# Optimization experiments

Hardware: AMD Instinct MI355X
Metric: run time of the kernel (lower is better)

## Reference

```python
import jax, jax.numpy as jnp
import numpy as np

B, N, C = 2, 2048, 1024
H = 16
HD = C // H  # 64


def setup_inputs() -> dict:
    key = jax.random.key(0)
    ks = jax.random.split(key, 6)
    x = jax.random.normal(ks[0], (B, N, C), dtype=jnp.float32)
    # realistic rotary angles
    inv_freq = 1.0 / (10000.0 ** (np.arange(0, HD, 2, dtype=np.float32) / HD))
    t = np.arange(N, dtype=np.float32)
    freqs = np.outer(t, inv_freq)                      # [N, HD/2]
    emb = np.concatenate([freqs, freqs], axis=-1)      # [N, HD]
    cos = jnp.asarray(np.cos(emb), dtype=jnp.float32)
    sin = jnp.asarray(np.sin(emb), dtype=jnp.float32)
    qkv_w = jax.random.normal(ks[1], (3 * C, C), dtype=jnp.float32) * (1.0 / np.sqrt(C))
    proj_w = jax.random.normal(ks[2], (C, C), dtype=jnp.float32) * (1.0 / np.sqrt(C))
    proj_b = jnp.zeros((C,), dtype=jnp.float32)
    return {"x": x, "cos": cos, "sin": sin, "qkv_w": qkv_w, "proj_w": proj_w, "proj_b": proj_b}


def _apply_rope(x, cos, sin):
    # x: [B, H, N, HD]; cos/sin: [N, HD] (broadcast over B, H)
    x1, x2 = jnp.split(x, 2, axis=-1)
    rotated = jnp.concatenate([-x2, x1], axis=-1)
    return x * cos + rotated * sin


def reference(x, cos, sin, qkv_w, proj_w, proj_b):
    b, n, c = x.shape
    scale = (c // H) ** (-0.5)
    qkv = jnp.einsum('bnc,dc->bnd', x, qkv_w)          # [B, N, 3C]
    qkv = qkv.reshape(b, n, 3, H, HD).transpose(2, 0, 3, 1, 4)  # [3, B, H, N, HD]
    q, k, v = qkv[0], qkv[1], qkv[2]
    q = _apply_rope(q, cos, sin)
    k = _apply_rope(k, cos, sin)
    attn = jnp.einsum('bhid,bhjd->bhij', q, k) * scale  # [B, H, N, N]
    attn = jax.nn.softmax(attn, axis=-1)
    out = jnp.einsum('bhij,bhjd->bhid', attn, v)        # [B, H, N, HD]
    out = out.transpose(0, 2, 1, 3).reshape(b, n, c)    # [B, N, C]
    return jnp.einsum('bnc,dc->bnd', out, proj_w) + proj_b
```

## Files before the change

### kernel.cpp

```cpp
#include <hip/hip_runtime.h>
#include <stdint.h>

typedef __bf16 bf16;
typedef bf16 bf16x8 __attribute__((ext_vector_type(8)));
typedef float f32x4 __attribute__((ext_vector_type(4)));
typedef float f32x16 __attribute__((ext_vector_type(16)));
typedef unsigned short u16x8 __attribute__((ext_vector_type(8)));
typedef unsigned short u16x4 __attribute__((ext_vector_type(4)));

__device__ __forceinline__ unsigned short f2bfu(float f) {
    union { bf16 h; unsigned short u; } x;
    x.h = (bf16)f;
    return x.u;
}
__device__ __forceinline__ float bfu2f(unsigned short u) {
    union { unsigned int i; float f; } x;
    x.i = ((unsigned int)u) << 16;
    return x.f;
}
__device__ __forceinline__ unsigned int pack2bf(float a, float b) {
    union { bf16 h[2]; unsigned int u; } x;
    x.h[0] = (bf16)a; x.h[1] = (bf16)b;
    return x.u;
}
__device__ __forceinline__ void pl32_swap(unsigned int &a, unsigned int &b) {
    asm volatile("v_permlane32_swap_b32 %0, %1" : "+v"(a), "+v"(b));
}

__device__ __forceinline__ void gld_lds16(const void* g, void* l) {
    __builtin_amdgcn_global_load_lds(
        (const __attribute__((address_space(1))) unsigned int*)(uintptr_t)g,
        (__attribute__((address_space(3))) unsigned int*)(unsigned int)(uintptr_t)l,
        16, 0, 0);
}

__global__ void cast_bf16_kernel(const float* __restrict__ in,
                                 unsigned short* __restrict__ out, int n8) {
    int i = blockIdx.x * blockDim.x + threadIdx.x;
    if (i >= n8) return;
    const f32x4* p = (const f32x4*)(in + (size_t)i * 8);
    f32x4 a = p[0], b = p[1];
    u16x8 o;
    o[0]=f2bfu(a[0]); o[1]=f2bfu(a[1]); o[2]=f2bfu(a[2]); o[3]=f2bfu(a[3]);
    o[4]=f2bfu(b[0]); o[5]=f2bfu(b[1]); o[6]=f2bfu(b[2]); o[7]=f2bfu(b[3]);
    *(u16x8*)(out + (size_t)i * 8) = o;
}

__global__ void rope_kernel(unsigned short* __restrict__ qkv,
                            const float* __restrict__ cosp,
                            const float* __restrict__ sinp) {
    int tid = blockIdx.x * blockDim.x + threadIdx.x;
    int i8  = tid & 3;
    int h   = (tid >> 2) & 15;
    int sel = (tid >> 6) & 1;
    int n   = (tid >> 7) & 2047;
    int b   = tid >> 18;
    size_t base = ((size_t)(b*2048 + n))*3072 + sel*1024 + h*64 + i8*8;
    u16x8 x1 = *(u16x8*)(qkv + base);
    u16x8 x2 = *(u16x8*)(qkv + base + 32);
    const f32x4* cp = (const f32x4*)(cosp + n*64 + i8*8);
    const f32x4* sp = (const f32x4*)(sinp + n*64 + i8*8);
    f32x4 c0 = cp[0], c1 = cp[1], s0 = sp[0], s1 = sp[1];
    float scale = sel ? 1.0f : (0.125f * 1.44269504088896f);
    u16x8 o1, o2;
#pragma unroll
    for (int j = 0; j < 8; j++) {
        float cc = (j < 4) ? c0[j] : c1[j-4];
        float ss = (j < 4) ? s0[j] : s1[j-4];
        float a = bfu2f(x1[j]), d = bfu2f(x2[j]);
        o1[j] = f2bfu((a*cc - d*ss) * scale);
        o2[j] = f2bfu((d*cc + a*ss) * scale);
    }
    *(u16x8*)(qkv + base)      = o1;
    *(u16x8*)(qkv + base + 32) = o2;
}

__global__ __launch_bounds__(512, 2) void gemm_qkv8(
    const unsigned short* __restrict__ A, const unsigned short* __restrict__ B,
    unsigned short* __restrict__ C, int M, int N, int K)
{
    extern __shared__ char smem[];
    int nwgx = gridDim.x;
    int nwg  = nwgx * gridDim.y;
    int orig = blockIdx.y * nwgx + blockIdx.x;
    int cpx  = nwg >> 3;
    int wg   = (orig & 7) * cpx + (orig >> 3);
    int bx = wg % nwgx, by = wg / nwgx;
    int m0 = by << 8, n0 = bx << 8;
    int t  = threadIdx.x;
    int wv = t >> 6, l = t & 63;
    int fr = l & 15, fq = l >> 4;
    int wm = (wv >> 2) << 7;
    int wn = (wv & 3) << 6;
    int aswz = (fr & 3) << 4;

    auto stage = [&](int kt, int bsel) {
        int k0 = kt << 5;
        char* base = smem + (bsel << 15);
#pragma unroll
        for (int j = 0; j < 2; ++j) {
            int y   = (j << 13) + t * 16;
            int ly  = y ^ (((y >> 6) & 3) << 4);
            int row = ly >> 6;
            int colu = (ly & 63) >> 1;
            gld_lds16(A + (size_t)(m0 + row) * K + k0 + colu,
                      base + ((j << 13) + (wv << 10)));
            gld_lds16(B + (size_t)(n0 + row) * K + k0 + colu,
                      base + 16384 + ((j << 13) + (wv << 10)));
        }
    };

    f32x4 acc[8][4];
#pragma unroll
    for (int m = 0; m < 8; ++m)
#pragma unroll
        for (int n = 0; n < 4; ++n) acc[m][n] = f32x4{0.f, 0.f, 0.f, 0.f};

    stage(0, 0);
    stage(1, 1);
    int cb = 0;
    for (int kt = 0; kt < 32; ++kt) {
        if (kt < 31) asm volatile("s_waitcnt vmcnt(4)" ::: "memory");
        else         asm volatile("s_waitcnt vmcnt(0)" ::: "memory");
        __builtin_amdgcn_s_barrier();
        if (kt + 2 < 32) {
            int sb = cb - 1; if (sb < 0) sb = 2;
            stage(kt + 2, sb);
        }
        const char* base = smem + (cb << 15);
        const char* Ab = base + ((wm + fr) << 6) + ((fq * 16) ^ aswz);
        const char* Bb = base + 16384 + ((wn + fr) << 6) + ((fq * 16) ^ aswz);
        bf16x8 bfr[4], af[4];
#pragma unroll
        for (int n = 0; n < 4; ++n) bfr[n] = *(const bf16x8*)(Bb + (n << 10));
#pragma unroll
        for (int m = 0; m < 4; ++m) af[m]  = *(const bf16x8*)(Ab + (m << 10));
        __builtin_amdgcn_s_barrier();
        __builtin_amdgcn_s_setprio(1);
#pragma unroll
        for (int m = 0; m < 4; ++m)
#pragma unroll
            for (int n = 0; n < 4; ++n)
                acc[m][n] = __builtin_amdgcn_mfma_f32_16x16x32_bf16(af[m], bfr[n], acc[m][n], 0, 0, 0);
        __builtin_amdgcn_s_setprio(0);
#pragma unroll
        for (int m = 0; m < 4; ++m) af[m] = *(const bf16x8*)(Ab + ((m + 4) << 10));
        __builtin_amdgcn_s_barrier();
        __builtin_amdgcn_s_setprio(1);
#pragma unroll
        for (int m = 0; m < 4; ++m)
#pragma unroll
            for (int n = 0; n < 4; ++n)
                acc[m + 4][n] = __builtin_amdgcn_mfma_f32_16x16x32_bf16(af[m], bfr[n], acc[m + 4][n], 0, 0, 0);
        __builtin_amdgcn_s_setprio(0);
        cb = (cb == 2) ? 0 : cb + 1;
    }
#pragma unroll
    for (int m = 0; m < 8; ++m)
#pragma unroll
        for (int n = 0; n < 4; ++n)
#pragma unroll
            for (int e = 0; e < 4; ++e) {
                int row = m0 + wm + m * 16 + fq * 4 + e;
                int col = n0 + wn + n * 16 + fr;
                C[(size_t)row * N + col] = f2bfu(acc[m][n][e]);
            }
}

template<int OUT_F32>
__global__ __launch_bounds__(256, 2) void gemm_bt(
    const unsigned short* __restrict__ A, const unsigned short* __restrict__ B,
    void* __restrict__ Cp, const float* __restrict__ bias,
    int M, int N, int K)
{
    __shared__ __align__(16) unsigned short As[2][128*32];
    __shared__ __align__(16) unsigned short Bs[2][128*32];
    int nwg  = gridDim.x * gridDim.y;
    int orig = blockIdx.y * gridDim.x + blockIdx.x;
    int qq = nwg >> 3, rr = nwg & 7;
    int xcd = orig & 7, idx = orig >> 3;
    int wg = (xcd < rr) ? (xcd*(qq+1) + idx) : (rr*(qq+1) + (xcd-rr)*qq + idx);
    int bx = wg % gridDim.x, by = wg / gridDim.x;
    int m0 = by * 128, n0 = bx * 128;
    int t = threadIdx.x;
    int w = t >> 6, l = t & 63;
    int c = l & 15, g = l >> 4;
    int wm = (w >> 1) * 64, wn = (w & 1) * 64;

    auto stage = [&](int kt, int bsel) {
#pragma unroll
        for (int r2 = 0; r2 < 2; ++r2) {
            int xb = w*2048 + r2*1024;
            int x  = xb + l*16;
            int row  = x >> 6;
            int colu = (x & 63) >> 1;
            int k0 = kt << 5;
            gld_lds16(A + (size_t)(m0+row)*K + k0 + colu, (void*)(As[bsel] + (xb >> 1)));
            gld_lds16(B + (size_t)(n0+row)*K + k0 + colu, (void*)(Bs[bsel] + (xb >> 1)));
        }
    };

    f32x4 acc[4][4];
#pragma unroll
    for (int i = 0; i < 4; i++)
#pragma unroll
        for (int j = 0; j < 4; j++) acc[i][j] = f32x4{0.f,0.f,0.f,0.f};

    int nkt = K >> 5;
    stage(0, 0);
    int cur = 0;
    for (int kt = 0; kt < nkt; ++kt) {
        __syncthreads();
        if (kt + 1 < nkt) stage(kt + 1, cur ^ 1);
        const unsigned short* Ab = As[cur] + wm*32;
        const unsigned short* Bb = Bs[cur] + wn*32;
        bf16x8 af[4], bfr[4];
#pragma unroll
        for (int i = 0; i < 4; i++) af[i]  = *(const bf16x8*)(Ab + (i*16+c)*32 + g*8);
#pragma unroll
        for (int i = 0; i < 4; i++) bfr[i] = *(const bf16x8*)(Bb + (i*16+c)*32 + g*8);
#pragma unroll
        for (int i = 0; i < 4; i++)
#pragma unroll
            for (int j = 0; j < 4; j++)
                acc[i][j] = __builtin_amdgcn_mfma_f32_16x16x32_bf16(af[i], bfr[j], acc[i][j], 0, 0, 0);
        cur ^= 1;
    }
#pragma unroll
    for (int i = 0; i < 4; i++)
#pragma unroll
        for (int j = 0; j < 4; j++)
#pragma unroll
            for (int e = 0; e < 4; e++) {
                int row = m0 + wm + i*16 + g*4 + e;
                int col = n0 + wn + j*16 + c;
                float v = acc[i][j][e];
                if (bias) v += bias[col];
                if (OUT_F32) ((float*)Cp)[(size_t)row*N + col] = v;
                else ((unsigned short*)Cp)[(size_t)row*N + col] = f2bfu(v);
            }
}

__global__ __launch_bounds__(512, 4) void attn_kernel(
    const unsigned short* __restrict__ qkv, unsigned short* __restrict__ outp)
{
    __shared__ __align__(16) char lds[65536];
    int bh = blockIdx.y;
    int b = bh >> 4, h = bh & 15;
    int q0 = blockIdx.x << 7;
    int t = threadIdx.x;
    int w = t >> 6, l = t & 63;
    int pair = w >> 2, wp = w & 3;
    int tp = t & 255;
    int q = l & 31, hi = l >> 5;
    int qw = q0 + wp*32;
    size_t bh_base = ((size_t)b*2048)*3072 + (size_t)h*64;

    auto kbase = [&](int bsel) -> char* { return lds + (((pair << 1) | bsel) << 13); };
    auto vbase = [&](int bsel) -> char* { return lds + 32768 + (((pair << 1) | bsel) << 13); };

    auto stageK = [&](int kv0, int bsel) {
#pragma unroll
        for (int r2 = 0; r2 < 2; ++r2) {
            int xb = wp*2048 + r2*1024;
            int x  = xb + l*16;
            int row  = x >> 7;
            int scolb = (x & 127) ^ ((row & 7) << 4);
            gld_lds16(qkv + bh_base + 1024 + (size_t)(kv0 + row)*3072 + (scolb >> 1),
                      kbase(bsel) + xb);
        }
    };
    auto loadV = [&](int kv0, u16x8 &v0, u16x8 &v1) {
        int p  = tp >> 3;
        int hb = (tp & 7) << 3;
        const unsigned short* src = qkv + bh_base + 2048 + (size_t)(kv0 + 2*p)*3072 + hb;
        v0 = *(const u16x8*)src;
        v1 = *(const u16x8*)(src + 3072);
    };
    auto writeV = [&](const u16x8 &v0, const u16x8 &v1, int bsel) {
        int p  = tp >> 3;
        int hb = (tp & 7) << 3;
        char* vb = vbase(bsel);
#pragma unroll
        for (int e = 0; e < 8; e++) {
            int hd = hb + e;
            int colb = (4*p) ^ ((((hd) ^ (hd >> 3)) & 7) << 4);
            *(unsigned int*)(vb + hd*128 + colb) =
                (unsigned int)v0[e] | ((unsigned int)v1[e] << 16);
        }
    };

    bf16x8 qf[4];
#pragma unroll
    for (int dc = 0; dc < 4; dc++)
        qf[dc] = *(const bf16x8*)(qkv + bh_base + (size_t)(qw + q)*3072 + dc*16 + hi*8);

    f32x16 oacc[2];
#pragma unroll
    for (int e = 0; e < 16; e++) { oacc[0][e] = 0.f; oacc[1][e] = 0.f; }
    float lsum = 0.f;

    int tile0 = pair << 4;
    u16x8 vc0, vc1, vn0, vn1;
    stageK(tile0 << 6, 0);
    loadV(tile0 << 6, vc0, vc1);
    int cur = 0;

    for (int it = 0; it < 16; ++it) {
        writeV(vc0, vc1, cur);
        __syncthreads();
        if (it < 15) {
            int kv0n = (tile0 + it + 1) << 6;
            stageK(kv0n, cur ^ 1);
            loadV(kv0n, vn0, vn1);
        }
        const char* ksb = kbase(cur);
        const char* vtb = vbase(cur);

#pragma unroll
        for (int sblk = 0; sblk < 2; ++sblk) {
            f32x16 st;
#pragma unroll
            for (int e = 0; e < 16; e++) st[e] = 0.f;
            int krow = sblk*32 + q;
            int ksw = (krow & 7) << 4;
#pragma unroll
            for (int dc = 0; dc < 4; ++dc) {
                bf16x8 kf = *(const bf16x8*)(ksb + krow*128 + ((dc*32 + hi*16) ^ ksw));
                st = __builtin_amdgcn_mfma_f32_32x32x16_bf16(kf, qf[dc], st, 0, 0, 0);
            }
            unsigned int wds[8];
#pragma unroll
            for (int m = 0; m < 8; m++) {
                float p0 = __builtin_amdgcn_exp2f(st[2*m]);
                float p1 = __builtin_amdgcn_exp2f(st[2*m+1]);
                lsum += p0 + p1;
                wds[m] = pack2bf(p0, p1);
            }
#pragma unroll
            for (int half = 0; half < 2; ++half) {
                unsigned int a0 = wds[half*4 + 0], b0 = wds[half*4 + 2];
                unsigned int a1 = wds[half*4 + 1], b1 = wds[half*4 + 3];
                pl32_swap(a0, b0);
                pl32_swap(a1, b1);
                union { unsigned int u[4]; bf16x8 v; } pf;
                pf.u[0] = a0; pf.u[1] = a1; pf.u[2] = b0; pf.u[3] = b1;
                int kc = sblk*2 + half;
#pragma unroll
                for (int hdblk = 0; hdblk < 2; ++hdblk) {
                    int hd = hdblk*32 + q;
                    int vsw = ((hd ^ (hd >> 3)) & 7) << 4;
                    bf16x8 vf = *(const bf16x8*)(vtb + hd*128 + ((kc*32 + hi*16) ^ vsw));
                    oacc[hdblk] = __builtin_amdgcn_mfma_f32_32x32x16_bf16(vf, pf.v, oacc[hdblk], 0, 0, 0);
                }
            }
        }
        vc0 = vn0; vc1 = vn1;
        cur ^= 1;
    }
    float lt = lsum + __shfl_xor(lsum, 32, 64);

    __syncthreads();
    int cbase = ((wp << 6) + l) << 7;
    int swl = (l & 7) << 4;
    if (pair == 1) {
#pragma unroll
        for (int j = 0; j < 8; ++j) {
            int hb = j >> 2, qd = j & 3;
            f32x4 v = f32x4{oacc[hb][qd*4+0], oacc[hb][qd*4+1],
                            oacc[hb][qd*4+2], oacc[hb][qd*4+3]};
            *(f32x4*)(lds + cbase + ((j << 4) ^ swl)) = v;
        }
        ((float*)(lds + 32768))[(wp << 6) + l] = lt;
    }
    __syncthreads();
    if (pair == 0) {
#pragma unroll
        for (int j = 0; j < 8; ++j) {
            int hb = j >> 2, qd = j & 3;
            f32x4 v = *(const f32x4*)(lds + cbase + ((j << 4) ^ swl));
#pragma unroll
            for (int e = 0; e < 4; ++e) oacc[hb][qd*4+e] += v[e];
        }
        lt += ((float*)(lds + 32768))[(wp << 6) + l];
        float rinv = 1.0f / lt;
        size_t orow = (size_t)(b*2048 + qw + q) * 1024 + h*64;
#pragma unroll
        for (int hdblk = 0; hdblk < 2; ++hdblk)
#pragma unroll
            for (int quad = 0; quad < 4; ++quad) {
                u16x4 o4;
#pragma unroll
                for (int j = 0; j < 4; j++)
                    o4[j] = f2bfu(oacc[hdblk][quad*4 + j] * rinv);
                *(u16x4*)(outp + orow + hdblk*32 + quad*8 + hi*4) = o4;
            }
    }
}

extern "C" void kernel_launch(void* const* d_in, const int* in_sizes, int n_in,
                              void* d_out, int out_size, void* d_ws, size_t ws_size,
                              hipStream_t stream) {
    const float* x      = (const float*)d_in[0];
    const float* cosp   = (const float*)d_in[1];
    const float* sinp   = (const float*)d_in[2];
    const float* qkv_w  = (const float*)d_in[3];
    const float* proj_w = (const float*)d_in[4];
    const float* proj_b = (const float*)d_in[5];

    char* ws = (char*)d_ws;
    unsigned short* xb     = (unsigned short*)(ws);
    unsigned short* wqkvb  = (unsigned short*)(ws + (size_t)(8u << 20));
    unsigned short* wprojb = (unsigned short*)(ws + (size_t)(14u << 20));
    unsigned short* qkvb   = (unsigned short*)(ws + (size_t)(16u << 20));
    unsigned short* attno  = xb;

    cast_bf16_kernel<<<2048, 256, 0, stream>>>(x, xb, 524288);
    cast_bf16_kernel<<<1536, 256, 0, stream>>>(qkv_w, wqkvb, 393216);
    cast_bf16_kernel<<<512, 256, 0, stream>>>(proj_w, wprojb, 131072);

    hipFuncSetAttribute((const void*)gemm_qkv8,
                        hipFuncAttributeMaxDynamicSharedMemorySize, 98304);
    gemm_qkv8<<<dim3(12, 16), 512, 98304, stream>>>(xb, wqkvb, qkvb, 4096, 3072, 1024);
    rope_kernel<<<2048, 256, 0, stream>>>(qkvb, cosp, sinp);
    attn_kernel<<<dim3(16, 32), 512, 0, stream>>>(qkvb, attno);
    gemm_bt<1><<<dim3(8, 32), 256, 0, stream>>>(attno, wprojb, d_out, proj_b, 4096, 1024, 1024);
}
```

Baseline: 132.6 us.

## Merge cast kernels, retile QKV GEMM to 256x128, swizzle LDS, add setprio

Replaces the three separate fp32-to-bf16 cast launches with a single kernel that selects its source by thread index. The QKV GEMM tile shrinks from 256x256 to 256x128, which doubles the grid to 384 workgroups, reduces LDS per block, and removes the second MFMA half-phase and its extra barrier. An XOR swizzle is added to the LDS staging and reads of the output-projection GEMM to reduce bank conflicts, and s_setprio hints are added around the MFMA blocks in the projection GEMM and the attention kernel. In exchange the QKV GEMM reuses each loaded A tile across a smaller N extent, so global traffic per FLOP rises.

```diff
diff --git a/kernel.cpp b/kernel.cpp
--- a/kernel.cpp
+++ b/kernel.cpp
@@ -34,16 +34,23 @@
         16, 0, 0);
 }
 
-__global__ void cast_bf16_kernel(const float* __restrict__ in,
-                                 unsigned short* __restrict__ out, int n8) {
+__global__ void cast3_kernel(const float* __restrict__ x,
+                             const float* __restrict__ w1,
+                             const float* __restrict__ w2,
+                             unsigned short* __restrict__ ox,
+                             unsigned short* __restrict__ o1,
+                             unsigned short* __restrict__ o2) {
     int i = blockIdx.x * blockDim.x + threadIdx.x;
-    if (i >= n8) return;
-    const f32x4* p = (const f32x4*)(in + (size_t)i * 8);
+    const float* in; unsigned short* out; int k;
+    if (i < 524288)       { in = x;  out = ox; k = i; }
+    else if (i < 917504)  { in = w1; out = o1; k = i - 524288; }
+    else                  { in = w2; out = o2; k = i - 917504; }
+    const f32x4* p = (const f32x4*)(in + (size_t)k * 8);
     f32x4 a = p[0], b = p[1];
     u16x8 o;
     o[0]=f2bfu(a[0]); o[1]=f2bfu(a[1]); o[2]=f2bfu(a[2]); o[3]=f2bfu(a[3]);
     o[4]=f2bfu(b[0]); o[5]=f2bfu(b[1]); o[6]=f2bfu(b[2]); o[7]=f2bfu(b[3]);
-    *(u16x8*)(out + (size_t)i * 8) = o;
+    *(u16x8*)(out + (size_t)k * 8) = o;
 }
 
 __global__ void rope_kernel(unsigned short* __restrict__ qkv,
@@ -75,7 +82,7 @@
     *(u16x8*)(qkv + base + 32) = o2;
 }
 
-__global__ __launch_bounds__(512, 2) void gemm_qkv8(
+__global__ __launch_bounds__(512, 2) void gemm_qkv8b(
     const unsigned short* __restrict__ A, const unsigned short* __restrict__ B,
     unsigned short* __restrict__ C, int M, int N, int K)
 {
@@ -86,56 +93,62 @@
     int cpx  = nwg >> 3;
     int wg   = (orig & 7) * cpx + (orig >> 3);
     int bx = wg % nwgx, by = wg / nwgx;
-    int m0 = by << 8, n0 = bx << 8;
+    int m0 = by << 8, n0 = bx << 7;
     int t  = threadIdx.x;
     int wv = t >> 6, l = t & 63;
     int fr = l & 15, fq = l >> 4;
-    int wm = (wv >> 2) << 7;
-    int wn = (wv & 3) << 6;
-    int aswz = (fr & 3) << 4;
+    int wm = (wv >> 1) << 6;
+    int wn = (wv & 1) << 6;
 
     auto stage = [&](int kt, int bsel) {
         int k0 = kt << 5;
-        char* base = smem + (bsel << 15);
+        char* base = smem + bsel * 24576;
 #pragma unroll
         for (int j = 0; j < 2; ++j) {
-            int y   = (j << 13) + t * 16;
-            int ly  = y ^ (((y >> 6) & 3) << 4);
-            int row = ly >> 6;
-            int colu = (ly & 63) >> 1;
+            int y  = (j << 13) + t * 16;
+            int ly = y ^ (((y >> 7) & 3) << 4);
+            int row = ly >> 6, colu = (ly & 63) >> 1;
             gld_lds16(A + (size_t)(m0 + row) * K + k0 + colu,
-                      base + ((j << 13) + (wv << 10)));
+                      base + (j << 13) + (wv << 10));
+        }
+        {
+            int y  = t * 16;
+            int ly = y ^ (((y >> 7) & 3) << 4);
+            int row = ly >> 6, colu = (ly & 63) >> 1;
             gld_lds16(B + (size_t)(n0 + row) * K + k0 + colu,
-                      base + 16384 + ((j << 13) + (wv << 10)));
+                      base + 16384 + (wv << 10));
         }
     };
 
-    f32x4 acc[8][4];
-#pragma unroll
-    for (int m = 0; m < 8; ++m)
-#pragma unroll
-        for (int n = 0; n < 4; ++n) acc[m][n] = f32x4{0.f, 0.f, 0.f, 0.f};
+    f32x4 acc[4][4];
+#pragma unroll
+    for (int i = 0; i < 4; i++)
+#pragma unroll
+        for (int j = 0; j < 4; j++) acc[i][j] = f32x4{0.f,0.f,0.f,0.f};
 
     stage(0, 0);
     stage(1, 1);
     int cb = 0;
     for (int kt = 0; kt < 32; ++kt) {
-        if (kt < 31) asm volatile("s_waitcnt vmcnt(4)" ::: "memory");
+        if (kt < 31) asm volatile("s_waitcnt vmcnt(3)" ::: "memory");
         else         asm volatile("s_waitcnt vmcnt(0)" ::: "memory");
         __builtin_amdgcn_s_barrier();
         if (kt + 2 < 32) {
             int sb = cb - 1; if (sb < 0) sb = 2;
             stage(kt + 2, sb);
         }
-        const char* base = smem + (cb << 15);
-        const char* Ab = base + ((wm + fr) << 6) + ((fq * 16) ^ aswz);
-        const char* Bb = base + 16384 + ((wn + fr) << 6) + ((fq * 16) ^ aswz);
-        bf16x8 bfr[4], af[4];
-#pragma unroll
-        for (int n = 0; n < 4; ++n) bfr[n] = *(const bf16x8*)(Bb + (n << 10));
-#pragma unroll
-        for (int m = 0; m < 4; ++m) af[m]  = *(const bf16x8*)(Ab + (m << 10));
-        __builtin_amdgcn_s_barrier();
+        const char* base = smem + cb * 24576;
+        bf16x8 af[4], bfr[4];
+#pragma unroll
+        for (int m = 0; m < 4; ++m) {
+            int row = wm + m*16 + fr;
+            af[m] = *(const bf16x8*)(base + row*64 + ((fq ^ ((row >> 1) & 3)) << 4));
+        }
+#pragma unroll
+        for (int n = 0; n < 4; ++n) {
+            int row = wn + n*16 + fr;
+            bfr[n] = *(const bf16x8*)(base + 16384 + row*64 + ((fq ^ ((row >> 1) & 3)) << 4));
+        }
         __builtin_amdgcn_s_setprio(1);
 #pragma unroll
         for (int m = 0; m < 4; ++m)
@@ -143,26 +156,16 @@
             for (int n = 0; n < 4; ++n)
                 acc[m][n] = __builtin_amdgcn_mfma_f32_16x16x32_bf16(af[m], bfr[n], acc[m][n], 0, 0, 0);
         __builtin_amdgcn_s_setprio(0);
-#pragma unroll
-        for (int m = 0; m < 4; ++m) af[m] = *(const bf16x8*)(Ab + ((m + 4) << 10));
-        __builtin_amdgcn_s_barrier();
-        __builtin_amdgcn_s_setprio(1);
-#pragma unroll
-        for (int m = 0; m < 4; ++m)
-#pragma unroll
-            for (int n = 0; n < 4; ++n)
-                acc[m + 4][n] = __builtin_amdgcn_mfma_f32_16x16x32_bf16(af[m], bfr[n], acc[m + 4][n], 0, 0, 0);
-        __builtin_amdgcn_s_setprio(0);
         cb = (cb == 2) ? 0 : cb + 1;
     }
 #pragma unroll
-    for (int m = 0; m < 8; ++m)
+    for (int m = 0; m < 4; ++m)
 #pragma unroll
         for (int n = 0; n < 4; ++n)
 #pragma unroll
             for (int e = 0; e < 4; ++e) {
-                int row = m0 + wm + m * 16 + fq * 4 + e;
-                int col = n0 + wn + n * 16 + fr;
+                int row = m0 + wm + m*16 + fq*4 + e;
+                int col = n0 + wn + n*16 + fr;
                 C[(size_t)row * N + col] = f2bfu(acc[m][n][e]);
             }
 }
@@ -192,8 +195,9 @@
         for (int r2 = 0; r2 < 2; ++r2) {
             int xb = w*2048 + r2*1024;
             int x  = xb + l*16;
-            int row  = x >> 6;
-            int colu = (x & 63) >> 1;
+            int lx = x ^ (((x >> 7) & 3) << 4);
+            int row  = lx >> 6;
+            int colu = (lx & 63) >> 1;
             int k0 = kt << 5;
             gld_lds16(A + (size_t)(m0+row)*K + k0 + colu, (void*)(As[bsel] + (xb >> 1)));
             gld_lds16(B + (size_t)(n0+row)*K + k0 + colu, (void*)(Bs[bsel] + (xb >> 1)));
@@ -212,18 +216,23 @@
     for (int kt = 0; kt < nkt; ++kt) {
         __syncthreads();
         if (kt + 1 < nkt) stage(kt + 1, cur ^ 1);
-        const unsigned short* Ab = As[cur] + wm*32;
-        const unsigned short* Bb = Bs[cur] + wn*32;
+        const char* Ab = (const char*)As[cur];
+        const char* Bb = (const char*)Bs[cur];
         bf16x8 af[4], bfr[4];
 #pragma unroll
-        for (int i = 0; i < 4; i++) af[i]  = *(const bf16x8*)(Ab + (i*16+c)*32 + g*8);
-#pragma unroll
-        for (int i = 0; i < 4; i++) bfr[i] = *(const bf16x8*)(Bb + (i*16+c)*32 + g*8);
+        for (int i = 0; i < 4; i++) {
+            int rowa = wm + i*16 + c;
+            int rowb = wn + i*16 + c;
+            af[i]  = *(const bf16x8*)(Ab + rowa*64 + ((g ^ ((rowa >> 1) & 3)) << 4));
+            bfr[i] = *(const bf16x8*)(Bb + rowb*64 + ((g ^ ((rowb >> 1) & 3)) << 4));
+        }
+        __builtin_amdgcn_s_setprio(1);
 #pragma unroll
         for (int i = 0; i < 4; i++)
 #pragma unroll
             for (int j = 0; j < 4; j++)
                 acc[i][j] = __builtin_amdgcn_mfma_f32_16x16x32_bf16(af[i], bfr[j], acc[i][j], 0, 0, 0);
+        __builtin_amdgcn_s_setprio(0);
         cur ^= 1;
     }
 #pragma unroll
@@ -324,11 +333,13 @@
             for (int e = 0; e < 16; e++) st[e] = 0.f;
             int krow = sblk*32 + q;
             int ksw = (krow & 7) << 4;
+            __builtin_amdgcn_s_setprio(1);
 #pragma unroll
             for (int dc = 0; dc < 4; ++dc) {
                 bf16x8 kf = *(const bf16x8*)(ksb + krow*128 + ((dc*32 + hi*16) ^ ksw));
                 st = __builtin_amdgcn_mfma_f32_32x32x16_bf16(kf, qf[dc], st, 0, 0, 0);
             }
+            __builtin_amdgcn_s_setprio(0);
             unsigned int wds[8];
 #pragma unroll
             for (int m = 0; m < 8; m++) {
@@ -346,6 +357,7 @@
                 union { unsigned int u[4]; bf16x8 v; } pf;
                 pf.u[0] = a0; pf.u[1] = a1; pf.u[2] = b0; pf.u[3] = b1;
                 int kc = sblk*2 + half;
+                __builtin_amdgcn_s_setprio(1);
 #pragma unroll
                 for (int hdblk = 0; hdblk < 2; ++hdblk) {
                     int hd = hdblk*32 + q;
@@ -353,6 +365,7 @@
                     bf16x8 vf = *(const bf16x8*)(vtb + hd*128 + ((kc*32 + hi*16) ^ vsw));
                     oacc[hdblk] = __builtin_amdgcn_mfma_f32_32x32x16_bf16(vf, pf.v, oacc[hdblk], 0, 0, 0);
                 }
+                __builtin_amdgcn_s_setprio(0);
             }
         }
         vc0 = vn0; vc1 = vn1;
@@ -415,13 +428,11 @@
     unsigned short* qkvb   = (unsigned short*)(ws + (size_t)(16u << 20));
     unsigned short* attno  = xb;
 
-    cast_bf16_kernel<<<2048, 256, 0, stream>>>(x, xb, 524288);
-    cast_bf16_kernel<<<1536, 256, 0, stream>>>(qkv_w, wqkvb, 393216);
-    cast_bf16_kernel<<<512, 256, 0, stream>>>(proj_w, wprojb, 131072);
-
-    hipFuncSetAttribute((const void*)gemm_qkv8,
-                        hipFuncAttributeMaxDynamicSharedMemorySize, 98304);
-    gemm_qkv8<<<dim3(12, 16), 512, 98304, stream>>>(xb, wqkvb, qkvb, 4096, 3072, 1024);
+    cast3_kernel<<<4096, 256, 0, stream>>>(x, qkv_w, proj_w, xb, wqkvb, wprojb);
+
+    hipFuncSetAttribute((const void*)gemm_qkv8b,
+                        hipFuncAttributeMaxDynamicSharedMemorySize, 73728);
+    gemm_qkv8b<<<dim3(24, 16), 512, 73728, stream>>>(xb, wqkvb, qkvb, 4096, 3072, 1024);
     rope_kernel<<<2048, 256, 0, stream>>>(qkvb, cosp, sinp);
     attn_kernel<<<dim3(16, 32), 512, 0, stream>>>(qkvb, attno);
     gemm_bt<1><<<dim3(8, 32), 256, 0, stream>>>(attno, wprojb, d_out, proj_b, 4096, 1024, 1024);
```

Result: faster. 123.4 us (-6.9%).
